# Kernel optimization log

Measured on AMD Instinct MI355X. Metric: run time of the kernel, lower is better.

The kernel has to match this reference:

```python
import jax, jax.numpy as jnp
import numpy as np
from jax import lax

B, T, D, H = 2048, 512, 88, 16


def setup_inputs() -> dict:
    key = jax.random.key(0)
    k1, k2, k3, k4 = jax.random.split(key, 4)
    # binary piano-roll observations [num_sequences, max_length, data_dim]
    sequences = (jax.random.uniform(k1, (B, T, D)) < 0.5).astype(jnp.float32)
    # simplex transition matrix [H, H]
    probs_x = jax.nn.softmax(jax.random.normal(k2, (H, H)), axis=-1)
    # unit-interval emission probs [H, D]
    probs_y = jax.nn.sigmoid(jax.random.normal(k3, (H, D)))
    lengths = jax.random.randint(k4, (B,), 1, T + 1).astype(jnp.int32)
    mb = jnp.arange(B, dtype=jnp.int64)
    mask = jnp.ones((B,), dtype=bool)
    scale = jnp.float32(1.0)
    return {"sequences": sequences, "probs_x": probs_x, "probs_y": probs_y,
            "scale": scale, "lengths": lengths, "mb": mb, "mask": mask}


def reference(sequences, probs_x, probs_y, scale, lengths, mb, mask):
    # Minibatch selection (mb indexes sequences/lengths, as in the pyro model)
    seq = sequences[mb]            # [B, T, D]
    lens = lengths[mb]             # [B]
    log_A = jnp.log(probs_x)       # [H, H] transition log-probs
    log_py = jnp.log(probs_y)      # [H, D]
    log_1mpy = jnp.log1p(-probs_y)
    # Bernoulli emission log-likelihood summed over tones plate: [B, T, H]
    emit = (jnp.einsum('btd,hd->bth', seq, log_py)
            + jnp.einsum('btd,hd->bth', 1.0 - seq, log_1mpy))
    NEG = jnp.float32(-1e30)
    # x starts at state 0 before the first transition -> delta at state 0
    alpha0 = jnp.full((seq.shape[0], log_A.shape[0]), NEG).at[:, 0].set(0.0)

    def step(alpha, inp):
        emit_t, t = inp            # emit_t: [B, H]
        nxt = jax.nn.logsumexp(alpha[:, :, None] + log_A[None], axis=1) + emit_t
        valid = (t < lens)[:, None]  # handlers.mask(t < lengths)
        return jnp.where(valid, nxt, alpha), None

    emit_tbh = jnp.swapaxes(emit, 0, 1)          # [T, B, H]
    alphaT, _ = lax.scan(step, alpha0, (emit_tbh, jnp.arange(emit_tbh.shape[0])))
    ll = jax.nn.logsumexp(alphaT, axis=-1)       # marginal log-lik per sequence
    # sequences-plate mask + handlers.scale
    return scale * jnp.where(mask, ll, 0.0)
```

## Files before the change

### kernel.cpp

```cpp
#include <hip/hip_runtime.h>

#define B_N 2048
#define T_N 512
#define D_N 88
#define H_N 16
#define NEGF (-1e30f)
#define LN2F 0.69314718055994530942f

typedef __attribute__((ext_vector_type(8))) short short8;
typedef __attribute__((ext_vector_type(4))) float floatx4;

template<int CTRL>
__device__ __forceinline__ float dppf(float x) {
    return __int_as_float(__builtin_amdgcn_update_dpp(
        0, __float_as_int(x), CTRL, 0xF, 0xF, false));
}

__device__ __forceinline__ float grp16_max(float v) {
    v = fmaxf(v, dppf<0x128>(v));
    v = fmaxf(v, dppf<0x124>(v));
    v = fmaxf(v, dppf<0x122>(v));
    v = fmaxf(v, dppf<0x121>(v));
    return v;
}
__device__ __forceinline__ float grp16_sum(float v) {
    v += dppf<0x128>(v);
    v += dppf<0x124>(v);
    v += dppf<0x122>(v);
    v += dppf<0x121>(v);
    return v;
}

__device__ __forceinline__ void calib(const float* __restrict__ px, int h,
                                      float (&aro)[16]) {
    float idxf = (float)h;
    aro[0]  = px[h * 16 + h];
    aro[1]  = px[((int)dppf<0x121>(idxf)) * 16 + h];
    aro[2]  = px[((int)dppf<0x122>(idxf)) * 16 + h];
    aro[3]  = px[((int)dppf<0x123>(idxf)) * 16 + h];
    aro[4]  = px[((int)dppf<0x124>(idxf)) * 16 + h];
    aro[5]  = px[((int)dppf<0x125>(idxf)) * 16 + h];
    aro[6]  = px[((int)dppf<0x126>(idxf)) * 16 + h];
    aro[7]  = px[((int)dppf<0x127>(idxf)) * 16 + h];
    aro[8]  = px[((int)dppf<0x128>(idxf)) * 16 + h];
    aro[9]  = px[((int)dppf<0x129>(idxf)) * 16 + h];
    aro[10] = px[((int)dppf<0x12A>(idxf)) * 16 + h];
    aro[11] = px[((int)dppf<0x12B>(idxf)) * 16 + h];
    aro[12] = px[((int)dppf<0x12C>(idxf)) * 16 + h];
    aro[13] = px[((int)dppf<0x12D>(idxf)) * 16 + h];
    aro[14] = px[((int)dppf<0x12E>(idxf)) * 16 + h];
    aro[15] = px[((int)dppf<0x12F>(idxf)) * 16 + h];
}

__device__ __forceinline__ float matvec16(float p, const float (&aro)[16]) {
    float a0 = p * aro[0];
    float a1 = dppf<0x121>(p) * aro[1];
    float a2 = dppf<0x122>(p) * aro[2];
    float a3 = dppf<0x123>(p) * aro[3];
    a0 += dppf<0x124>(p) * aro[4];
    a1 += dppf<0x125>(p) * aro[5];
    a2 += dppf<0x126>(p) * aro[6];
    a3 += dppf<0x127>(p) * aro[7];
    a0 += dppf<0x128>(p) * aro[8];
    a1 += dppf<0x129>(p) * aro[9];
    a2 += dppf<0x12A>(p) * aro[10];
    a3 += dppf<0x12B>(p) * aro[11];
    a0 += dppf<0x12C>(p) * aro[12];
    a1 += dppf<0x12D>(p) * aro[13];
    a2 += dppf<0x12E>(p) * aro[14];
    a3 += dppf<0x12F>(p) * aro[15];
    return (a0 + a1) + (a2 + a3);
}

__device__ __forceinline__ void scan_step(float& aRel, float& M, float ec,
                                          float cval, bool valid,
                                          const float (&aro)[16]) {
    float p = exp2f(aRel);
    float s = matvec16(p, aro);
    float g = __log2f(s) + ec;
    if (valid) { aRel = g; M += cval; }
}

__device__ __forceinline__ void hmm_step(float& aRel, float& M, float emit2,
                                         bool valid, const float (&aro)[16]) {
    float p = exp2f(aRel);
    float s = matvec16(p, aro);
    float g = __log2f(s) + emit2;
    float mg = grp16_max(g);
    if (valid) { aRel = g - mg; M = M + mg; }
}

__global__ void hmm_prep(const float* __restrict__ probs_y,
                         ushort* __restrict__ bpack, float* __restrict__ base) {
    int tid = threadIdx.x;
    for (int i = tid; i < 3 * 64 * 8; i += 256) {
        int k = i >> 9;
        int l = (i >> 3) & 63;
        int j = i & 7;
        int kk = k * 32 + ((l >> 4) * 8) + j;
        int h = l & 15;
        ushort v = 0;
        if (kk < D_N) {
            float p = probs_y[h * D_N + kk];
            float lw = log2f(p) - log2f(1.0f - p);
            unsigned u = __float_as_uint(lw);
            u += 0x7FFFu + ((u >> 16) & 1u);
            v = (ushort)(u >> 16);
        }
        bpack[i] = v;
    }
    if (tid < H_N) {
        float s = 0.0f;
        for (int d = 0; d < D_N; ++d)
            s += log2f(1.0f - probs_y[tid * D_N + d]);
        base[tid] = s;
    }
}

__global__ __launch_bounds__(256) void hmm_emit(
    const float* __restrict__ seq, const int* __restrict__ lengths,
    const ushort* __restrict__ bpack, const float* __restrict__ base,
    float* __restrict__ ecBuf, float* __restrict__ cBuf) {
    int bid = blockIdx.x;
    int b = bid >> 3;
    int t0 = (bid & 7) * 64;
    if (t0 >= lengths[b]) return;

    __shared__ ushort sA[64 * 104];
    int tid = threadIdx.x;
    const float* gseq = seq + ((size_t)b * T_N + t0) * D_N;

    for (int f = tid; f < 768; f += 256) {
        if (f < 704) {
            int r = f / 11;
            int c = f - r * 11;
            const float* gp = gseq + f * 8;
            float4 v0 = *(const float4*)(gp);
            float4 v1 = *(const float4*)(gp + 4);
            uint4 w;
            w.x = (__float_as_uint(v0.x) >> 16) | (__float_as_uint(v0.y) & 0xFFFF0000u);
            w.y = (__float_as_uint(v0.z) >> 16) | (__float_as_uint(v0.w) & 0xFFFF0000u);
            w.z = (__float_as_uint(v1.x) >> 16) | (__float_as_uint(v1.y) & 0xFFFF0000u);
            w.w = (__float_as_uint(v1.z) >> 16) | (__float_as_uint(v1.w) & 0xFFFF0000u);
            *(uint4*)(&sA[r * 104 + c * 8]) = w;
        } else {
            int r = f - 704;
            uint4 z; z.x = 0; z.y = 0; z.z = 0; z.w = 0;
            *(uint4*)(&sA[r * 104 + 88]) = z;
        }
    }
    __syncthreads();

    int l = tid & 63, w = tid >> 6;
    int q = l >> 4, h = l & 15;

    const short8* bp = (const short8*)bpack;
    short8 bf0 = bp[l];
    short8 bf1 = bp[64 + l];
    short8 bf2 = bp[128 + l];

    int arow = w * 16 + h;
    short8 af0 = *(const short8*)&sA[arow * 104 + 0  + q * 8];
    short8 af1 = *(const short8*)&sA[arow * 104 + 32 + q * 8];
    short8 af2 = *(const short8*)&sA[arow * 104 + 64 + q * 8];

    floatx4 acc = {0.f, 0.f, 0.f, 0.f};
    acc = __builtin_amdgcn_mfma_f32_16x16x32_bf16(af0, bf0, acc, 0, 0, 0);
    acc = __builtin_amdgcn_mfma_f32_16x16x32_bf16(af1, bf1, acc, 0, 0, 0);
    acc = __builtin_amdgcn_mfma_f32_16x16x32_bf16(af2, bf2, acc, 0, 0, 0);

    float bh = base[h];
    float e0 = acc[0] + bh, e1 = acc[1] + bh, e2 = acc[2] + bh, e3 = acc[3] + bh;
    float c0 = grp16_max(e0), c1 = grp16_max(e1);
    float c2 = grp16_max(e2), c3 = grp16_max(e3);

    int tloc = t0 + w * 16 + q * 4;
    float4 ecv; ecv.x = e0 - c0; ecv.y = e1 - c1; ecv.z = e2 - c2; ecv.w = e3 - c3;
    *(float4*)&ecBuf[((size_t)(b * H_N + h)) * T_N + tloc] = ecv;
    if (h == 0) {
        float4 cv; cv.x = c0; cv.y = c1; cv.z = c2; cv.w = c3;
        *(float4*)&cBuf[(size_t)b * T_N + tloc] = cv;
    }
}

__global__ __launch_bounds__(64) void hmm_scan(
    const float* __restrict__ probs_x, const float* __restrict__ ecBuf,
    const float* __restrict__ cBuf, const int* __restrict__ lengths,
    const float* __restrict__ scale, float* __restrict__ out) {
    int lane = threadIdx.x;
    int sl = lane >> 4, h = lane & 15;
    int b0 = blockIdx.x * 4;
    int b = b0 + sl;
    int len = lengths[b];

    float aro[16];
    calib(probs_x, h, aro);

    int wmax = max(max(lengths[b0], lengths[b0 + 1]),
                   max(lengths[b0 + 2], lengths[b0 + 3]));

    const float4* eb = (const float4*)(ecBuf + ((size_t)(b * H_N + h)) * T_N);
    const float4* cb = (const float4*)(cBuf + (size_t)b * T_N);
    float aRel = (h == 0) ? 0.0f : NEGF;
    float M = 0.0f;

    int nch = (wmax + 3) >> 2;
    float4 e0 = eb[0], e1 = eb[1];
    float4 g0 = cb[0], g1 = cb[1];
    for (int c = 0; c < nch; ++c) {
        float4 e2 = eb[c + 2];
        float4 g2 = cb[c + 2];
        int t0c = c * 4;
        scan_step(aRel, M, e0.x, g0.x, t0c + 0 < len, aro);
        scan_step(aRel, M, e0.y, g0.y, t0c + 1 < len, aro);
        scan_step(aRel, M, e0.z, g0.z, t0c + 2 < len, aro);
        scan_step(aRel, M, e0.w, g0.w, t0c + 3 < len, aro);
        float mg = grp16_max(aRel);
        aRel -= mg; M += mg;
        e0 = e1; e1 = e2; g0 = g1; g1 = g2;
    }
    float pf = exp2f(aRel);
    float s = grp16_sum(pf);
    if (h == 0)
        out[b] = scale[0] * (LN2F * (M + __log2f(s)));
}

__global__ __launch_bounds__(64) void hmm_fused_naive(
    const float* __restrict__ seq, const float* __restrict__ px,
    const float* __restrict__ py, const float* __restrict__ sc,
    const int* __restrict__ lengths, float* __restrict__ out) {
    int lane = threadIdx.x;
    int sl = lane >> 4, h = lane & 15;
    int b0 = blockIdx.x * 4;
    int b = b0 + sl;
    int len = lengths[b];

    float aro[16];
    calib(px, h, aro);

    float wreg[88];
    float b2 = 0.0f;
#pragma unroll
    for (int d = 0; d < D_N; ++d) {
        float p = py[h * D_N + d];
        float l1 = log2f(1.0f - p);
        wreg[d] = log2f(p) - l1;
        b2 += l1;
    }
    int wmax = max(max(lengths[b0], lengths[b0 + 1]),
                   max(lengths[b0 + 2], lengths[b0 + 3]));

    float aRel = (h == 0) ? 0.0f : NEGF;
    float M = 0.0f;
    for (int t = 0; t < wmax; ++t) {
        const float4* sp = (const float4*)(seq + ((size_t)b * T_N + t) * D_N);
        float e = b2;
#pragma unroll
        for (int j = 0; j < 22; ++j) {
            float4 v = sp[j];
            e += v.x * wreg[4 * j] + v.y * wreg[4 * j + 1] +
                 v.z * wreg[4 * j + 2] + v.w * wreg[4 * j + 3];
        }
        hmm_step(aRel, M, e, t < len, aro);
    }
    float pf = exp2f(aRel);
    float s = grp16_sum(pf);
    if (h == 0)
        out[b] = sc[0] * (LN2F * (M + __log2f(s)));
}

extern "C" void kernel_launch(void* const* d_in, const int* in_sizes, int n_in,
                              void* d_out, int out_size, void* d_ws,
                              size_t ws_size, hipStream_t stream) {
    const float* seq = (const float*)d_in[0];
    const float* px  = (const float*)d_in[1];
    const float* py  = (const float*)d_in[2];
    const float* sc  = (const float*)d_in[3];
    const int*   len = (const int*)d_in[4];
    float* out = (float*)d_out;

    size_t ec_elems = (size_t)B_N * H_N * T_N;
    size_t c_elems  = (size_t)B_N * T_N;
    size_t need = (ec_elems + c_elems + 16) * sizeof(float) + 1536 * sizeof(ushort);
    if (ws_size >= need) {
        float*  ecBuf = (float*)d_ws;
        float*  cBuf  = ecBuf + ec_elems;
        float*  base  = cBuf + c_elems;
        ushort* bpack = (ushort*)(base + 16);
        hmm_prep<<<1, 256, 0, stream>>>(py, bpack, base);
        hmm_emit<<<B_N * 8, 256, 0, stream>>>(seq, len, bpack, base, ecBuf, cBuf);
        hmm_scan<<<B_N / 4, 64, 0, stream>>>(px, ecBuf, cBuf, len, sc, out);
    } else {
        hmm_fused_naive<<<B_N / 4, 64, 0, stream>>>(seq, px, py, sc, len, out);
    }
}
```

Before: 545.4 us.

## Run scan in linear domain with bf16 precomputed emission weights

The emit kernel now stores exp2 of the normalized emission log-likelihoods as bf16 instead of fp32 logs. This halves the intermediate buffer traffic. The scan kernel keeps alpha in the linear domain, multiplying the matvec result by the emission weight. That removes the per-step exp2/log2 pair from the serial dependency chain, with renormalization done every 4 steps through exponent-bit scaling. The cost is reduced precision from bf16 weights and a possible underflow risk between renormalizations.

```diff
diff --git a/kernel.cpp b/kernel.cpp
--- a/kernel.cpp
+++ b/kernel.cpp
@@ -29,6 +29,12 @@
     v += dppf<0x122>(v);
     v += dppf<0x121>(v);
     return v;
+}
+
+__device__ __forceinline__ ushort bf16rne(float f) {
+    unsigned u = __float_as_uint(f);
+    u += 0x7FFFu + ((u >> 16) & 1u);
+    return (ushort)(u >> 16);
 }
 
 __device__ __forceinline__ void calib(const float* __restrict__ px, int h,
@@ -72,15 +78,6 @@
     return (a0 + a1) + (a2 + a3);
 }
 
-__device__ __forceinline__ void scan_step(float& aRel, float& M, float ec,
-                                          float cval, bool valid,
-                                          const float (&aro)[16]) {
-    float p = exp2f(aRel);
-    float s = matvec16(p, aro);
-    float g = __log2f(s) + ec;
-    if (valid) { aRel = g; M += cval; }
-}
-
 __device__ __forceinline__ void hmm_step(float& aRel, float& M, float emit2,
                                          bool valid, const float (&aro)[16]) {
     float p = exp2f(aRel);
@@ -102,10 +99,7 @@
         ushort v = 0;
         if (kk < D_N) {
             float p = probs_y[h * D_N + kk];
-            float lw = log2f(p) - log2f(1.0f - p);
-            unsigned u = __float_as_uint(lw);
-            u += 0x7FFFu + ((u >> 16) & 1u);
-            v = (ushort)(u >> 16);
+            v = bf16rne(log2f(p) - log2f(1.0f - p));
         }
         bpack[i] = v;
     }
@@ -120,7 +114,7 @@
 __global__ __launch_bounds__(256) void hmm_emit(
     const float* __restrict__ seq, const int* __restrict__ lengths,
     const ushort* __restrict__ bpack, const float* __restrict__ base,
-    float* __restrict__ ecBuf, float* __restrict__ cBuf) {
+    ushort* __restrict__ wBuf, float* __restrict__ cBuf) {
     int bid = blockIdx.x;
     int b = bid >> 3;
     int t0 = (bid & 7) * 64;
@@ -175,8 +169,12 @@
     float c2 = grp16_max(e2), c3 = grp16_max(e3);
 
     int tloc = t0 + w * 16 + q * 4;
-    float4 ecv; ecv.x = e0 - c0; ecv.y = e1 - c1; ecv.z = e2 - c2; ecv.w = e3 - c3;
-    *(float4*)&ecBuf[((size_t)(b * H_N + h)) * T_N + tloc] = ecv;
+    ushort4 wv;
+    wv.x = bf16rne(exp2f(e0 - c0));
+    wv.y = bf16rne(exp2f(e1 - c1));
+    wv.z = bf16rne(exp2f(e2 - c2));
+    wv.w = bf16rne(exp2f(e3 - c3));
+    *(ushort4*)&wBuf[((size_t)(b * H_N + h)) * T_N + tloc] = wv;
     if (h == 0) {
         float4 cv; cv.x = c0; cv.y = c1; cv.z = c2; cv.w = c3;
         *(float4*)&cBuf[(size_t)b * T_N + tloc] = cv;
@@ -184,7 +182,7 @@
 }
 
 __global__ __launch_bounds__(64) void hmm_scan(
-    const float* __restrict__ probs_x, const float* __restrict__ ecBuf,
+    const float* __restrict__ probs_x, const ushort* __restrict__ wBuf,
     const float* __restrict__ cBuf, const int* __restrict__ lengths,
     const float* __restrict__ scale, float* __restrict__ out) {
     int lane = threadIdx.x;
@@ -199,30 +197,37 @@
     int wmax = max(max(lengths[b0], lengths[b0 + 1]),
                    max(lengths[b0 + 2], lengths[b0 + 3]));
 
-    const float4* eb = (const float4*)(ecBuf + ((size_t)(b * H_N + h)) * T_N);
-    const float4* cb = (const float4*)(cBuf + (size_t)b * T_N);
-    float aRel = (h == 0) ? 0.0f : NEGF;
+    const ushort4* eb = (const ushort4*)(wBuf + ((size_t)(b * H_N + h)) * T_N);
+    const float4*  cb = (const float4*)(cBuf + (size_t)b * T_N);
+    float aLin = (h == 0) ? 1.0f : 0.0f;
     float M = 0.0f;
 
     int nch = (wmax + 3) >> 2;
-    float4 e0 = eb[0], e1 = eb[1];
-    float4 g0 = cb[0], g1 = cb[1];
+    ushort4 wA = eb[0], wB = eb[1], wC = eb[2];
+    float4  cA = cb[0], cB = cb[1], cC = cb[2];
     for (int c = 0; c < nch; ++c) {
-        float4 e2 = eb[c + 2];
-        float4 g2 = cb[c + 2];
+        ushort4 wD = eb[c + 3];
+        float4  cD = cb[c + 3];
+        float f0 = __uint_as_float((unsigned)wA.x << 16);
+        float f1 = __uint_as_float((unsigned)wA.y << 16);
+        float f2 = __uint_as_float((unsigned)wA.z << 16);
+        float f3 = __uint_as_float((unsigned)wA.w << 16);
         int t0c = c * 4;
-        scan_step(aRel, M, e0.x, g0.x, t0c + 0 < len, aro);
-        scan_step(aRel, M, e0.y, g0.y, t0c + 1 < len, aro);
-        scan_step(aRel, M, e0.z, g0.z, t0c + 2 < len, aro);
-        scan_step(aRel, M, e0.w, g0.w, t0c + 3 < len, aro);
-        float mg = grp16_max(aRel);
-        aRel -= mg; M += mg;
-        e0 = e1; e1 = e2; g0 = g1; g1 = g2;
-    }
-    float pf = exp2f(aRel);
-    float s = grp16_sum(pf);
+        float s;
+        s = matvec16(aLin, aro); if (t0c + 0 < len) { aLin = s * f0; M += cA.x; }
+        s = matvec16(aLin, aro); if (t0c + 1 < len) { aLin = s * f1; M += cA.y; }
+        s = matvec16(aLin, aro); if (t0c + 2 < len) { aLin = s * f2; M += cA.z; }
+        s = matvec16(aLin, aro); if (t0c + 3 < len) { aLin = s * f3; M += cA.w; }
+        float mx = grp16_max(aLin);
+        unsigned ex = (__float_as_uint(mx) >> 23) & 0xFFu;
+        aLin *= __uint_as_float((254u - ex) << 23);
+        M += (float)((int)ex - 127);
+        wA = wB; wB = wC; wC = wD;
+        cA = cB; cB = cC; cC = cD;
+    }
+    float ssum = grp16_sum(aLin);
     if (h == 0)
-        out[b] = scale[0] * (LN2F * (M + __log2f(s)));
+        out[b] = scale[0] * (LN2F * (M + __log2f(ssum)));
 }
 
 __global__ __launch_bounds__(64) void hmm_fused_naive(
@@ -279,17 +284,17 @@
     const int*   len = (const int*)d_in[4];
     float* out = (float*)d_out;
 
-    size_t ec_elems = (size_t)B_N * H_N * T_N;
-    size_t c_elems  = (size_t)B_N * T_N;
-    size_t need = (ec_elems + c_elems + 16) * sizeof(float) + 1536 * sizeof(ushort);
+    size_t w_elems = (size_t)B_N * H_N * T_N;
+    size_t c_elems = (size_t)B_N * T_N;
+    size_t need = w_elems * 2 + c_elems * 4 + 16 * 4 + 1536 * 2 + 256;
     if (ws_size >= need) {
-        float*  ecBuf = (float*)d_ws;
-        float*  cBuf  = ecBuf + ec_elems;
+        ushort* wBuf  = (ushort*)d_ws;
+        float*  cBuf  = (float*)(wBuf + w_elems);
         float*  base  = cBuf + c_elems;
         ushort* bpack = (ushort*)(base + 16);
         hmm_prep<<<1, 256, 0, stream>>>(py, bpack, base);
-        hmm_emit<<<B_N * 8, 256, 0, stream>>>(seq, len, bpack, base, ecBuf, cBuf);
-        hmm_scan<<<B_N / 4, 64, 0, stream>>>(px, ecBuf, cBuf, len, sc, out);
+        hmm_emit<<<B_N * 8, 256, 0, stream>>>(seq, len, bpack, base, wBuf, cBuf);
+        hmm_scan<<<B_N / 4, 64, 0, stream>>>(px, wBuf, cBuf, len, sc, out);
     } else {
         hmm_fused_naive<<<B_N / 4, 64, 0, stream>>>(seq, px, py, sc, len, out);
     }
```

Result: faster. 528.8 us (-3.1%).
